# Performance work log

Hardware: AMD Instinct MI355X
Metric: run time of the kernel (lower is better)

The kernel has to match this reference:

```python
import jax, jax.numpy as jnp
import numpy as np

B, T, DM, DK = 16, 2048, 1024, 128

def setup_inputs() -> dict:
    key = jax.random.key(0)
    k1, k2, k3, k4 = jax.random.split(key, 4)
    x = jax.random.normal(k1, (B, T, DM), dtype=jnp.float32)
    # Linear(dm, dk, bias=False) weights, stored as [dm, dk] for x @ W
    scale = 1.0 / np.sqrt(DM)
    W_q = jax.random.normal(k2, (DM, DK), dtype=jnp.float32) * scale
    W_k = jax.random.normal(k3, (DM, DK), dtype=jnp.float32) * scale
    W_v = jax.random.normal(k4, (DM, DK), dtype=jnp.float32) * scale
    return {"x": x, "W_q": W_q, "W_k": W_k, "W_v": W_v}

def reference(x, W_q, W_k, W_v):
    # q, k, v: [B, T, DK]
    q = jnp.einsum('btd,dk->btk', x, W_q)
    k = jnp.einsum('btd,dk->btk', x, W_k)
    v = jnp.einsum('btd,dk->btk', x, W_v)
    dk = k.shape[-1]
    # scores: [B, T, T], scaled by dk**-0.5
    wei = jnp.einsum('bqk,bsk->bqs', q, k) * (dk ** -0.5)
    # causal mask (tril == 0 -> -inf)
    causal = jnp.tril(jnp.ones((q.shape[1], q.shape[1]), dtype=bool))
    wei = jnp.where(causal, wei, -jnp.inf)
    wei = jax.nn.softmax(wei, axis=-1)
    out = jnp.einsum('bqs,bsk->bqk', wei, v)  # [B, T, DK]
    return out
```

## Files before the change

kernel.cpp:

```cpp
#include <hip/hip_runtime.h>
#include <hip/hip_bf16.h>

#define NB 16
#define NT 2048
#define NDM 1024
#define NDK 128

typedef __bf16 bf16;
typedef bf16 bf16x4 __attribute__((ext_vector_type(4)));
typedef bf16 bf16x8 __attribute__((ext_vector_type(8)));
typedef float f32x4 __attribute__((ext_vector_type(4)));

__device__ inline bf16 to_bf16(float f) {
    __hip_bfloat16 h = __float2bfloat16(f);
    return *reinterpret_cast<bf16*>(&h);
}

__global__ __launch_bounds__(256) void transpose_w_kernel(
        const float* __restrict__ Wq, const float* __restrict__ Wk,
        const float* __restrict__ Wv, bf16* __restrict__ Wt) {
    int idx = blockIdx.x * 256 + threadIdx.x;
    int w = idx >> 17;
    int r = idx & (NDM * NDK - 1);
    int k = r >> 7;
    int n = r & (NDK - 1);
    const float* W = (w == 0) ? Wq : ((w == 1) ? Wk : Wv);
    Wt[(size_t)w * NDK * NDM + (size_t)n * NDM + k] = to_bf16(W[(size_t)k * NDK + n]);
}

__global__ __launch_bounds__(256) void proj_kernel(
        const float* __restrict__ x, const bf16* __restrict__ Wt,
        bf16* __restrict__ qkv, bf16* __restrict__ Vt) {
    __shared__ __align__(16) char smem[128 * 136 * 2];
    bf16 (*As)[40] = reinterpret_cast<bf16(*)[40]>(smem);
    bf16 (*Bs)[40] = reinterpret_cast<bf16(*)[40]>(smem + 10240);
    bf16 (*Tl)[136] = reinterpret_cast<bf16(*)[136]>(smem);

    const int tid = threadIdx.x;
    const int lane = tid & 63;
    const int wave = tid >> 6;
    const int wr = wave >> 1, wc = wave & 1;
    const int r16 = lane & 15, kg = lane >> 4;
    const int mb = blockIdx.x;
    const int w = blockIdx.y;
    const float* xA = x + (size_t)mb * 128 * NDM;
    const bf16* Bt = Wt + (size_t)w * NDK * NDM;

    f32x4 acc[4][4];
#pragma unroll
    for (int m = 0; m < 4; m++)
#pragma unroll
        for (int n = 0; n < 4; n++) acc[m][n] = (f32x4){0.f, 0.f, 0.f, 0.f};

    for (int k0 = 0; k0 < NDM; k0 += 32) {
#pragma unroll
        for (int p = 0; p < 4; p++) {
            int row = p * 32 + (tid >> 3);
            int c4 = (tid & 7) * 4;
            const float4 v = *reinterpret_cast<const float4*>(&xA[(size_t)row * NDM + k0 + c4]);
            bf16x4 bv = { to_bf16(v.x), to_bf16(v.y), to_bf16(v.z), to_bf16(v.w) };
            *reinterpret_cast<bf16x4*>(&As[row][c4]) = bv;
        }
#pragma unroll
        for (int p = 0; p < 2; p++) {
            int idx = (p * 256 + tid) * 8;
            int n = idx >> 5;
            int kk = idx & 31;
            *reinterpret_cast<bf16x8*>(&Bs[n][kk]) =
                *reinterpret_cast<const bf16x8*>(&Bt[(size_t)n * NDM + k0 + kk]);
        }
        __syncthreads();
        bf16x8 af[4], bfr[4];
#pragma unroll
        for (int m = 0; m < 4; m++)
            af[m] = *reinterpret_cast<const bf16x8*>(&As[wr * 64 + m * 16 + r16][kg * 8]);
#pragma unroll
        for (int n = 0; n < 4; n++)
            bfr[n] = *reinterpret_cast<const bf16x8*>(&Bs[wc * 64 + n * 16 + r16][kg * 8]);
#pragma unroll
        for (int m = 0; m < 4; m++)
#pragma unroll
            for (int n = 0; n < 4; n++)
                acc[m][n] = __builtin_amdgcn_mfma_f32_16x16x32_bf16(af[m], bfr[n], acc[m][n], 0, 0, 0);
        __syncthreads();
    }

    if (w < 2) {
        bf16* outw = qkv + (size_t)w * (size_t)(NB * NT) * NDK;
#pragma unroll
        for (int m = 0; m < 4; m++) {
            int rowb = mb * 128 + wr * 64 + m * 16 + kg * 4;
#pragma unroll
            for (int n = 0; n < 4; n++) {
                int col = wc * 64 + n * 16 + r16;
#pragma unroll
                for (int r = 0; r < 4; r++)
                    outw[(size_t)(rowb + r) * NDK + col] = to_bf16(acc[m][n][r]);
            }
        }
    } else {
#pragma unroll
        for (int m = 0; m < 4; m++) {
            int tl = wr * 64 + m * 16 + kg * 4;
#pragma unroll
            for (int n = 0; n < 4; n++) {
                int d = wc * 64 + n * 16 + r16;
                bf16x4 pv = { to_bf16(acc[m][n][0]), to_bf16(acc[m][n][1]),
                              to_bf16(acc[m][n][2]), to_bf16(acc[m][n][3]) };
                *reinterpret_cast<bf16x4*>(&Tl[d][tl]) = pv;
            }
        }
        __syncthreads();
        const int b = mb >> 4;
        const int t0 = (mb & 15) * 128;
        bf16* Vb = Vt + (size_t)b * NDK * NT;
#pragma unroll
        for (int p = 0; p < 8; p++) {
            int idx = p * 256 + tid;
            int d = idx >> 4, c = idx & 15;
            *reinterpret_cast<bf16x8*>(&Vb[(size_t)d * NT + t0 + c * 8]) =
                *reinterpret_cast<const bf16x8*>(&Tl[d][c * 8]);
        }
    }
}

__global__ __launch_bounds__(256) void attn_kernel(
        const bf16* __restrict__ Q, const bf16* __restrict__ K,
        const bf16* __restrict__ Vt, float* __restrict__ out) {
    __shared__ bf16 Ks[2][64][128];
    __shared__ bf16 Vs[2][128][64];
    __shared__ bf16 Ps[4][16][72];
    const int tid = threadIdx.x, lane = tid & 63, wave = tid >> 6;
    const int r16 = lane & 15, kg = lane >> 4;

    const int bid = blockIdx.x;
    const int xcd = bid & 7;
    const int j = bid >> 3;
    const int b = xcd * 2 + (j & 1);
    const int qb = (NT / 64 - 1) - (j >> 1);
    const int q0 = qb * 64;
    const size_t baseB = (size_t)b * NT * NDK;
    const size_t baseVt = (size_t)b * NDK * NT;

    const float scale = 0.08838834764831843f;
    bf16x8 qf[4];
    const int qglob = q0 + wave * 16 + r16;
#pragma unroll
    for (int kc = 0; kc < 4; kc++) {
        bf16x8 raw = *reinterpret_cast<const bf16x8*>(&Q[baseB + (size_t)qglob * NDK + kc * 32 + kg * 8]);
#pragma unroll
        for (int jj = 0; jj < 8; jj++) raw[jj] = to_bf16((float)raw[jj] * scale);
        qf[kc] = raw;
    }

    f32x4 o[8];
#pragma unroll
    for (int n = 0; n < 8; n++) o[n] = (f32x4){0.f, 0.f, 0.f, 0.f};
    float mrun = -INFINITY;
    float lrun = 0.f;

    int krow[4], kcol[4], vrow[4], vcol[4];
#pragma unroll
    for (int i = 0; i < 4; i++) {
        int idx = i * 256 + tid;
        krow[i] = idx >> 4; kcol[i] = idx & 15;
        vrow[i] = idx >> 3; vcol[i] = idx & 7;
    }

    const int nsteps = qb + 1;
    bf16x8 kreg[4], vreg[4];
#pragma unroll
    for (int i = 0; i < 4; i++) {
        kreg[i] = *reinterpret_cast<const bf16x8*>(&K[baseB + (size_t)krow[i] * NDK + kcol[i] * 8]);
        vreg[i] = *reinterpret_cast<const bf16x8*>(&Vt[baseVt + (size_t)vrow[i] * NT + vcol[i] * 8]);
    }
#pragma unroll
    for (int i = 0; i < 4; i++) {
        *reinterpret_cast<bf16x8*>(&Ks[0][krow[i]][(kcol[i] ^ (krow[i] & 7)) * 8]) = kreg[i];
        *reinterpret_cast<bf16x8*>(&Vs[0][vrow[i]][(vcol[i] ^ (vrow[i] & 7)) * 8]) = vreg[i];
    }
    if (nsteps > 1) {
#pragma unroll
        for (int i = 0; i < 4; i++) {
            kreg[i] = *reinterpret_cast<const bf16x8*>(&K[baseB + (size_t)(64 + krow[i]) * NDK + kcol[i] * 8]);
            vreg[i] = *reinterpret_cast<const bf16x8*>(&Vt[baseVt + (size_t)vrow[i] * NT + 64 + vcol[i] * 8]);
        }
    }
    __syncthreads();

    for (int s = 0; s < nsteps; s++) {
        const int cur = s & 1;
        const int kv0 = s * 64;

        f32x4 sfr[4];
#pragma unroll
        for (int n = 0; n < 4; n++) sfr[n] = (f32x4){0.f, 0.f, 0.f, 0.f};
#pragma unroll
        for (int n = 0; n < 4; n++) {
            const int krw = n * 16 + r16;
#pragma unroll
            for (int kc = 0; kc < 4; kc++) {
                bf16x8 kf = *reinterpret_cast<const bf16x8*>(&Ks[cur][krw][((kc * 4 + kg) ^ (krw & 7)) * 8]);
                sfr[n] = __builtin_amdgcn_mfma_f32_16x16x32_bf16(kf, qf[kc], sfr[n], 0, 0, 0);
            }
        }

        if (s == nsteps - 1) {
#pragma unroll
            for (int n = 0; n < 4; n++)
#pragma unroll
                for (int r = 0; r < 4; r++)
                    if (kv0 + n * 16 + kg * 4 + r > qglob) sfr[n][r] = -INFINITY;
        }

        float pm = -INFINITY;
#pragma unroll
        for (int n = 0; n < 4; n++) {
            float t0 = fmaxf(fmaxf(sfr[n][0], sfr[n][1]), fmaxf(sfr[n][2], sfr[n][3]));
            pm = fmaxf(pm, t0);
        }
        pm = fmaxf(pm, __shfl_xor(pm, 16, 64));
        pm = fmaxf(pm, __shfl_xor(pm, 32, 64));

        if (__any(pm > mrun)) {
            float mnew = fmaxf(mrun, pm);
            float corr = __expf(mrun - mnew);
            mrun = mnew;
            lrun *= corr;
            float co[4];
#pragma unroll
            for (int r = 0; r < 4; r++) co[r] = __shfl(corr, kg * 4 + r, 64);
#pragma unroll
            for (int n = 0; n < 8; n++)
#pragma unroll
                for (int r = 0; r < 4; r++) o[n][r] *= co[r];
        }

        float ps = 0.f;
#pragma unroll
        for (int n = 0; n < 4; n++) {
            bf16x4 pw;
#pragma unroll
            for (int r = 0; r < 4; r++) {
                float pv = __expf(sfr[n][r] - mrun);
                ps += pv;
                pw[r] = to_bf16(pv);
            }
            *reinterpret_cast<bf16x4*>(&Ps[wave][r16][n * 16 + kg * 4]) = pw;
        }
        ps += __shfl_xor(ps, 16, 64);
        ps += __shfl_xor(ps, 32, 64);
        lrun += ps;

#pragma unroll
        for (int kc2 = 0; kc2 < 2; kc2++) {
            bf16x8 pf = *reinterpret_cast<const bf16x8*>(&Ps[wave][r16][kc2 * 32 + kg * 8]);
#pragma unroll
            for (int n = 0; n < 8; n++) {
                const int vrw = n * 16 + r16;
                bf16x8 vf = *reinterpret_cast<const bf16x8*>(&Vs[cur][vrw][((kc2 * 4 + kg) ^ (vrw & 7)) * 8]);
                o[n] = __builtin_amdgcn_mfma_f32_16x16x32_bf16(pf, vf, o[n], 0, 0, 0);
            }
        }

        if (s + 1 < nsteps) {
#pragma unroll
            for (int i = 0; i < 4; i++) {
                *reinterpret_cast<bf16x8*>(&Ks[1 - cur][krow[i]][(kcol[i] ^ (krow[i] & 7)) * 8]) = kreg[i];
                *reinterpret_cast<bf16x8*>(&Vs[1 - cur][vrow[i]][(vcol[i] ^ (vrow[i] & 7)) * 8]) = vreg[i];
            }
            if (s + 2 < nsteps) {
                const int kv2 = (s + 2) * 64;
#pragma unroll
                for (int i = 0; i < 4; i++) {
                    kreg[i] = *reinterpret_cast<const bf16x8*>(&K[baseB + (size_t)(kv2 + krow[i]) * NDK + kcol[i] * 8]);
                    vreg[i] = *reinterpret_cast<const bf16x8*>(&Vt[baseVt + (size_t)vrow[i] * NT + kv2 + vcol[i] * 8]);
                }
            }
        }
        __syncthreads();
    }

    float linv = 1.0f / lrun;
    float li[4];
#pragma unroll
    for (int r = 0; r < 4; r++) li[r] = __shfl(linv, kg * 4 + r, 64);
#pragma unroll
    for (int n = 0; n < 8; n++)
#pragma unroll
        for (int r = 0; r < 4; r++) {
            int row = q0 + wave * 16 + kg * 4 + r;
            int col = n * 16 + r16;
            out[baseB + (size_t)row * NDK + col] = o[n][r] * li[r];
        }
}

extern "C" void kernel_launch(void* const* d_in, const int* in_sizes, int n_in,
                              void* d_out, int out_size, void* d_ws, size_t ws_size,
                              hipStream_t stream) {
    const float* x  = (const float*)d_in[0];
    const float* Wq = (const float*)d_in[1];
    const float* Wk = (const float*)d_in[2];
    const float* Wv = (const float*)d_in[3];
    float* out = (float*)d_out;

    char* ws = (char*)d_ws;
    bf16* Wt  = (bf16*)ws;
    bf16* qkv = (bf16*)(ws + (1ull << 20));
    bf16* Vtg = (bf16*)(ws + (26ull << 20));

    transpose_w_kernel<<<(3 * NDM * NDK) / 256, 256, 0, stream>>>(Wq, Wk, Wv, Wt);

    dim3 g1((NB * NT) / 128, 3);
    proj_kernel<<<g1, 256, 0, stream>>>(x, Wt, qkv, Vtg);

    bf16* Qp = qkv;
    bf16* Kp = qkv + (size_t)(NB * NT) * NDK;

    attn_kernel<<<dim3((NT / 64) * NB), 256, 0, stream>>>(Qp, Kp, Vtg, out);
}
```

Measured before the change: 101.9 us.

## Double-buffer projection GEMM with direct-to-LDS weight loads and swizzled layout

Rewrites the projection GEMM main loop into a two-stage software pipeline. The x tile is prefetched into registers one step ahead, and the weight tile is loaded straight into LDS with global_load_lds using an XOR-swizzled layout. Explicit vmcnt/lgkmcnt waits and a single barrier per step replace the two __syncthreads. This aims to hide global-load latency behind MFMA work and cut barrier stalls, at the cost of more LDS, more registers and fragile hand-managed wait counts.

```diff
diff --git a/kernel.cpp b/kernel.cpp
--- a/kernel.cpp
+++ b/kernel.cpp
@@ -15,6 +15,16 @@
     __hip_bfloat16 h = __float2bfloat16(f);
     return *reinterpret_cast<bf16*>(&h);
 }
+
+__device__ inline void gload_lds16(const void* g, void* l) {
+    __builtin_amdgcn_global_load_lds(
+        (const __attribute__((address_space(1))) unsigned int*)g,
+        (__attribute__((address_space(3))) unsigned int*)l, 16, 0, 0);
+}
+
+#define VMCNT(n) asm volatile("s_waitcnt vmcnt(" #n ")" ::: "memory")
+#define LGKM0()  asm volatile("s_waitcnt lgkmcnt(0)" ::: "memory")
+#define SCHEDB() __builtin_amdgcn_sched_barrier(0)
 
 __global__ __launch_bounds__(256) void transpose_w_kernel(
         const float* __restrict__ Wq, const float* __restrict__ Wk,
@@ -28,17 +38,12 @@
     Wt[(size_t)w * NDK * NDM + (size_t)n * NDM + k] = to_bf16(W[(size_t)k * NDK + n]);
 }
 
-__global__ __launch_bounds__(256) void proj_kernel(
+__global__ __launch_bounds__(256, 4) void proj_kernel(
         const float* __restrict__ x, const bf16* __restrict__ Wt,
         bf16* __restrict__ qkv, bf16* __restrict__ Vt) {
-    __shared__ __align__(16) char smem[128 * 136 * 2];
-    bf16 (*As)[40] = reinterpret_cast<bf16(*)[40]>(smem);
-    bf16 (*Bs)[40] = reinterpret_cast<bf16(*)[40]>(smem + 10240);
-    bf16 (*Tl)[136] = reinterpret_cast<bf16(*)[136]>(smem);
-
+    __shared__ __align__(16) char smem[36864];
     const int tid = threadIdx.x;
-    const int lane = tid & 63;
-    const int wave = tid >> 6;
+    const int lane = tid & 63, wave = tid >> 6;
     const int wr = wave >> 1, wc = wave & 1;
     const int r16 = lane & 15, kg = lane >> 4;
     const int mb = blockIdx.x;
@@ -46,45 +51,93 @@
     const float* xA = x + (size_t)mb * 128 * NDM;
     const bf16* Bt = Wt + (size_t)w * NDK * NDM;
 
+    auto AS = [&](int b) -> bf16* { return (bf16*)(smem + b * 10240); };
+    auto BS = [&](int b) -> bf16* { return (bf16*)(smem + 20480 + b * 8192); };
+
+    const int a_row = tid >> 1;
+    const int a_cb = (tid & 1) * 16;
+    float4 araw[4];
+    auto loadA = [&](int kt) {
+        const float* p = xA + (size_t)a_row * NDM + kt * 32 + a_cb;
+#pragma unroll
+        for (int i = 0; i < 4; i++) araw[i] = *reinterpret_cast<const float4*>(p + i * 4);
+    };
+    auto writeA = [&](int buf) {
+        bf16* dst = AS(buf) + a_row * 40 + a_cb;
+#pragma unroll
+        for (int h = 0; h < 2; h++) {
+            const float4 lo = araw[2 * h], hi = araw[2 * h + 1];
+            bf16x8 v;
+            v[0] = to_bf16(lo.x); v[1] = to_bf16(lo.y); v[2] = to_bf16(lo.z); v[3] = to_bf16(lo.w);
+            v[4] = to_bf16(hi.x); v[5] = to_bf16(hi.y); v[6] = to_bf16(hi.z); v[7] = to_bf16(hi.w);
+            *reinterpret_cast<bf16x8*>(dst + h * 8) = v;
+        }
+    };
+    auto stageB = [&](int buf, int kt) {
+#pragma unroll
+        for (int p = 0; p < 2; p++) {
+            int cid = p * 256 + tid;
+            int row = cid >> 2, c = cid & 3;
+            int cs = c ^ (row & 3);
+            gload_lds16(Bt + (size_t)row * NDM + kt * 32 + cs * 8,
+                        BS(buf) + (size_t)(p * 256 + wave * 64) * 8);
+        }
+    };
+
     f32x4 acc[4][4];
 #pragma unroll
     for (int m = 0; m < 4; m++)
 #pragma unroll
         for (int n = 0; n < 4; n++) acc[m][n] = (f32x4){0.f, 0.f, 0.f, 0.f};
 
-    for (int k0 = 0; k0 < NDM; k0 += 32) {
-#pragma unroll
-        for (int p = 0; p < 4; p++) {
-            int row = p * 32 + (tid >> 3);
-            int c4 = (tid & 7) * 4;
-            const float4 v = *reinterpret_cast<const float4*>(&xA[(size_t)row * NDM + k0 + c4]);
-            bf16x4 bv = { to_bf16(v.x), to_bf16(v.y), to_bf16(v.z), to_bf16(v.w) };
-            *reinterpret_cast<bf16x4*>(&As[row][c4]) = bv;
-        }
-#pragma unroll
-        for (int p = 0; p < 2; p++) {
-            int idx = (p * 256 + tid) * 8;
-            int n = idx >> 5;
-            int kk = idx & 31;
-            *reinterpret_cast<bf16x8*>(&Bs[n][kk]) =
-                *reinterpret_cast<const bf16x8*>(&Bt[(size_t)n * NDM + k0 + kk]);
-        }
-        __syncthreads();
+    loadA(0); SCHEDB();
+    stageB(0, 0); SCHEDB();
+    VMCNT(2);
+    writeA(0);
+    loadA(1); SCHEDB();
+    VMCNT(4);
+    LGKM0();
+    __builtin_amdgcn_s_barrier();
+    SCHEDB();
+    stageB(1, 1); SCHEDB();
+
+    for (int kt = 0; kt < 32; kt++) {
+        const int cur = kt & 1;
         bf16x8 af[4], bfr[4];
 #pragma unroll
         for (int m = 0; m < 4; m++)
-            af[m] = *reinterpret_cast<const bf16x8*>(&As[wr * 64 + m * 16 + r16][kg * 8]);
-#pragma unroll
-        for (int n = 0; n < 4; n++)
-            bfr[n] = *reinterpret_cast<const bf16x8*>(&Bs[wc * 64 + n * 16 + r16][kg * 8]);
+            af[m] = *reinterpret_cast<const bf16x8*>(AS(cur) + (wr * 64 + m * 16 + r16) * 40 + kg * 8);
+#pragma unroll
+        for (int n = 0; n < 4; n++) {
+            int br = wc * 64 + n * 16 + r16;
+            bfr[n] = *reinterpret_cast<const bf16x8*>(BS(cur) + br * 32 + ((kg ^ (br & 3)) * 8));
+        }
+        __builtin_amdgcn_s_setprio(1);
 #pragma unroll
         for (int m = 0; m < 4; m++)
 #pragma unroll
             for (int n = 0; n < 4; n++)
                 acc[m][n] = __builtin_amdgcn_mfma_f32_16x16x32_bf16(af[m], bfr[n], acc[m][n], 0, 0, 0);
-        __syncthreads();
-    }
-
+        __builtin_amdgcn_s_setprio(0);
+
+        if (kt + 1 < 32) {
+            SCHEDB();
+            VMCNT(2);
+            writeA(1 - cur);
+            if (kt + 2 < 32) {
+                loadA(kt + 2); SCHEDB();
+                VMCNT(4);
+            } else {
+                VMCNT(0);
+            }
+            LGKM0();
+            __builtin_amdgcn_s_barrier();
+            SCHEDB();
+            if (kt + 2 < 32) { stageB(cur, kt + 2); SCHEDB(); }
+        }
+    }
+
+    __syncthreads();
     if (w < 2) {
         bf16* outw = qkv + (size_t)w * (size_t)(NB * NT) * NDK;
 #pragma unroll
@@ -99,6 +152,7 @@
             }
         }
     } else {
+        bf16 (*Tl)[136] = reinterpret_cast<bf16(*)[136]>(smem);
 #pragma unroll
         for (int m = 0; m < 4; m++) {
             int tl = wr * 64 + m * 16 + kg * 4;
@@ -311,7 +365,7 @@
 
     transpose_w_kernel<<<(3 * NDM * NDK) / 256, 256, 0, stream>>>(Wq, Wk, Wv, Wt);
 
-    dim3 g1((NB * NT) / 128, 3);
+    dim3 g1(256, 3);
     proj_kernel<<<g1, 256, 0, stream>>>(x, Wt, qkv, Vtg);
 
     bf16* Qp = qkv;
```

New measurement: 110.0 us. 1.08x slower.
